# Kernel optimization log

Hardware: AMD Instinct MI355X
Metric: run time of the kernel (lower is better)

Reference implementation:

```python
import jax, jax.numpy as jnp
import numpy as np

C1, C2, BIG_K, STRIDE = 256, 256, 13, 1
EPS = 1e-5  # BatchNorm2d default


def setup_inputs() -> dict:
    key = jax.random.key(0)
    k1, k2, k3, k4, k5 = jax.random.split(key, 5)
    x = jax.random.normal(k1, (16, C1, 56, 56), dtype=jnp.float32)
    # Conv2d weight: (out_ch, in_ch, kH, kW), kaiming-ish scale
    w = jax.random.normal(k2, (C2, C1, BIG_K, BIG_K), dtype=jnp.float32) * (1.0 / np.sqrt(C1 * BIG_K * BIG_K))
    gamma = jax.random.uniform(k3, (C2,), dtype=jnp.float32, minval=0.5, maxval=1.5)
    beta = jax.random.normal(k4, (C2,), dtype=jnp.float32) * 0.1
    running_mean = jnp.zeros((C2,), dtype=jnp.float32)
    running_var = jax.random.uniform(k5, (C2,), dtype=jnp.float32, minval=0.5, maxval=1.5)
    return {"x": x, "w": w, "gamma": gamma, "beta": beta,
            "running_mean": running_mean, "running_var": running_var}


def reference(x, w, gamma, beta, running_mean, running_var):
    # Dense big_k x big_k conv fallback: Conv2d(c1, c2, 13, stride=1, pad=6, bias=False)
    pad = BIG_K // 2
    y = jax.lax.conv_general_dilated(
        x, w,
        window_strides=(STRIDE, STRIDE),
        padding=[(pad, pad), (pad, pad)],
        dimension_numbers=("NCHW", "OIHW", "NCHW"),
    )
    # BatchNorm2d (inference mode: running stats)
    inv = jax.lax.rsqrt(running_var + EPS)
    y = (y - running_mean[None, :, None, None]) * (gamma * inv)[None, :, None, None] + beta[None, :, None, None]
    # SiLU activation
    return y * jax.nn.sigmoid(y)
```

## Files before the change

kernel.cpp:

```cpp
#include <hip/hip_runtime.h>
#include <hip/hip_bf16.h>

#define C1c 256
#define C2c 256
#define NBAT 16
#define HH 56
#define WW 56
#define KS 13
#define PADc 6
#define HP 68
#define NPIX (NBAT*HH*WW)
#define PIXTILES 196
#define KSTEPS2 1352

typedef __bf16 bf16;
typedef bf16 bf16x8 __attribute__((ext_vector_type(8)));
typedef float floatx4 __attribute__((ext_vector_type(4)));

#define XT_ELEMS ((size_t)NBAT*HP*HP*C1c)
#define WT_ELEMS ((size_t)KSTEPS2*256*32)

__global__ __launch_bounds__(256) void xform_x(const float* __restrict__ x,
                                               bf16* __restrict__ xT) {
  __shared__ bf16 tile[56][258];
  const int tid = threadIdx.x;
  const int n = blockIdx.x / HP;
  const int hp = blockIdx.x - n * HP;
  const int ih = hp - PADc;
  const size_t pos_base = (size_t)(n * HP + hp) * HP * C1c;

  if (ih < 0 || ih >= HH) {
#pragma unroll 1
    for (int i = tid; i < HP * 32; i += 256) {
      int wp = i >> 5, g = i & 31;
      *(uint4*)(xT + pos_base + wp * C1c + g * 8) = (uint4){0u, 0u, 0u, 0u};
    }
    return;
  }

  const int wave = tid >> 6, lane = tid & 63;
#pragma unroll 4
  for (int i = 0; i < 64; ++i) {
    int c = i * 4 + wave;
    if (lane < WW) {
      float v = x[(((size_t)n * C1c + c) * HH + ih) * WW + lane];
      tile[lane][c] = (bf16)v;
    }
  }
  __syncthreads();

#pragma unroll 1
  for (int i = tid; i < HP * 32; i += 256) {
    int wp = i >> 5, g = i & 31;
    int iw = wp - PADc;
    uint4 o;
    if (iw >= 0 && iw < WW) {
      const uint* lp = (const uint*)&tile[iw][g * 8];
      o.x = lp[0]; o.y = lp[1]; o.z = lp[2]; o.w = lp[3];
    } else {
      o = (uint4){0u, 0u, 0u, 0u};
    }
    *(uint4*)(xT + pos_base + wp * C1c + g * 8) = o;
  }
}

__global__ __launch_bounds__(256) void xform_w(const float* __restrict__ w,
                                               bf16* __restrict__ wT) {
  int j = blockIdx.x * 256 + threadIdx.x;
  int part = j & 3;
  int c2 = (j >> 2) & 255;
  int kk = j >> 10;
  int kw = kk % 13;
  int t = kk / 13;
  int q = t & 7;
  int kh = t >> 3;
  int c1 = q * 32 + part * 8;
  const float* wp = w + ((size_t)c2 * C1c + c1) * (KS * KS) + kh * KS + kw;
  bf16x8 v;
#pragma unroll
  for (int i = 0; i < 8; i++) v[i] = (bf16)wp[(size_t)i * KS * KS];
  *(bf16x8*)(wT + (size_t)j * 8) = v;
}

__device__ __forceinline__ void gload_lds16(const bf16* g, bf16* l) {
  __builtin_amdgcn_global_load_lds(
      (const __attribute__((address_space(1))) void*)(g),
      (__attribute__((address_space(3))) void*)(l),
      16, 0, 0);
}

__global__ __launch_bounds__(512, 2) void conv_mfma(
    const bf16* __restrict__ xT, const bf16* __restrict__ wT,
    const float* __restrict__ gamma, const float* __restrict__ beta,
    const float* __restrict__ rmean, const float* __restrict__ rvar,
    float* __restrict__ out) {
  __shared__ __attribute__((aligned(16))) bf16 As[3][256 * 32];
  __shared__ __attribute__((aligned(16))) bf16 Bs[3][256 * 32];
  __shared__ float sS[256];
  __shared__ float sB[256];

  const int tid = threadIdx.x;
  const int lane = tid & 63;
  const int wave = tid >> 6;
  const int wm = wave >> 2, wn = wave & 3;

  const int orig = blockIdx.x;
  const int xcd = orig & 7, kb = orig >> 3;
  const int pixt = (xcd < 4 ? xcd * 25 : 100 + (xcd - 4) * 24) + kb;
  const int pixbase = pixt * 256;

  if (tid < 256) {
    float s = gamma[tid] * rsqrtf(rvar[tid] + 1e-5f);
    sS[tid] = s;
    sB[tid] = beta[tid] - rmean[tid] * s;
  }
  __syncthreads();

  const int part = tid & 3;
  const int row0 = tid >> 2;
  const int srcg = (part ^ ((row0 >> 1) & 3)) * 8;

  const int aOff0 = row0 * 32 + srcg;
  const int aOff1 = aOff0 + 128 * 32;

  int pOff0, pOff1;
  {
    int pix = pixbase + row0;
    int n = pix / (HH * WW);
    int rr = pix - n * (HH * WW);
    int oh = rr / WW;
    int ow = rr - oh * WW;
    pOff0 = ((n * HP + oh) * HP + ow) * C1c + srcg;
    pix += 128;
    n = pix / (HH * WW);
    rr = pix - n * (HH * WW);
    oh = rr / WW;
    ow = rr - oh * WW;
    pOff1 = ((n * HP + oh) * HP + ow) * C1c + srcg;
  }

  const int ldsA0 = wave * 512;

  const int mrow = lane & 15;
  const int kq = lane >> 4;
  const int g0 = (kq ^ ((mrow >> 1) & 3)) * 8;
  const int aRB = (wm * 128 + mrow) * 32 + g0;
  const int bRB = (wn * 64 + mrow) * 32 + g0;

  floatx4 acc[8][4];
#pragma unroll
  for (int mi = 0; mi < 8; mi++)
#pragma unroll
    for (int ni = 0; ni < 4; ni++) acc[mi][ni] = (floatx4){0.f, 0.f, 0.f, 0.f};

  gload_lds16(wT + aOff0, &As[0][ldsA0]);
  gload_lds16(wT + aOff1, &As[0][4096 + ldsA0]);
  gload_lds16(xT + pOff0, &Bs[0][ldsA0]);
  gload_lds16(xT + pOff1, &Bs[0][4096 + ldsA0]);
  gload_lds16(wT + 8192 + aOff0, &As[1][ldsA0]);
  gload_lds16(wT + 8192 + aOff1, &As[1][4096 + ldsA0]);
  gload_lds16(xT + pOff0 + C1c, &Bs[1][ldsA0]);
  gload_lds16(xT + pOff1 + C1c, &Bs[1][4096 + ldsA0]);
  asm volatile("s_waitcnt vmcnt(4)" ::: "memory");
  __builtin_amdgcn_s_barrier();

  int kwn = 2, qn = 0, khn = 0;
  const bf16* aPre = wT + 2 * 8192;

  auto do_step = [&](const bf16* Ac, const bf16* Bc, bf16* An, bf16* Bn) {

    bf16x8 af[8], bfr[4];
#pragma unroll
    for (int mi = 0; mi < 4; mi++)
      af[mi] = *(const bf16x8*)(Ac + aRB + mi * 512);
#pragma unroll
    for (int ni = 0; ni < 4; ni++)
      bfr[ni] = *(const bf16x8*)(Bc + bRB + ni * 512);
    gload_lds16(aPre + aOff0, An + ldsA0);
    gload_lds16(aPre + aOff1, An + 4096 + ldsA0);
    __builtin_amdgcn_sched_barrier(0);
    __builtin_amdgcn_s_barrier();
    __builtin_amdgcn_sched_barrier(0);
    __builtin_amdgcn_s_setprio(1);
#pragma unroll
    for (int mi = 0; mi < 4; mi++)
#pragma unroll
      for (int ni = 0; ni < 4; ni++)
        acc[mi][ni] = __builtin_amdgcn_mfma_f32_16x16x32_bf16(
            af[mi], bfr[ni], acc[mi][ni], 0, 0, 0);
    __builtin_amdgcn_s_setprio(0);

#pragma unroll
    for (int mi = 4; mi < 8; mi++)
      af[mi] = *(const bf16x8*)(Ac + aRB + mi * 512);
    int bOn = (khn * HP + kwn) * C1c + qn * 32;
    gload_lds16(xT + pOff0 + bOn, Bn + ldsA0);
    gload_lds16(xT + pOff1 + bOn, Bn + 4096 + ldsA0);
    kwn++; aPre += 8192;
    if (kwn == 13) {
      kwn = 0; qn++;
      if (qn == 8) {
        qn = 0; khn++;
        if (khn == 13) { khn = 0; aPre = wT; }
      }
    }
    __builtin_amdgcn_sched_barrier(0);
    __builtin_amdgcn_s_barrier();
    __builtin_amdgcn_sched_barrier(0);
    __builtin_amdgcn_s_setprio(1);
#pragma unroll
    for (int mi = 4; mi < 8; mi++)
#pragma unroll
      for (int ni = 0; ni < 4; ni++)
        acc[mi][ni] = __builtin_amdgcn_mfma_f32_16x16x32_bf16(
            af[mi], bfr[ni], acc[mi][ni], 0, 0, 0);
    __builtin_amdgcn_s_setprio(0);

    asm volatile("s_waitcnt vmcnt(4)" ::: "memory");
    __builtin_amdgcn_s_barrier();
  };

#pragma unroll 1
  for (int kk = 0; kk < KSTEPS2 - 2; kk += 3) {
    do_step(As[0], Bs[0], As[2], Bs[2]);
    do_step(As[1], Bs[1], As[0], Bs[0]);
    do_step(As[2], Bs[2], As[1], Bs[1]);
  }
  do_step(As[0], Bs[0], As[2], Bs[2]);
  do_step(As[1], Bs[1], As[0], Bs[0]);

  const int colL = lane & 15;
  const int quad = lane >> 4;
#pragma unroll
  for (int ni = 0; ni < 4; ni++) {
    int pix = pixbase + wn * 64 + ni * 16 + colL;
    int n = pix / (HH * WW);
    int rr = pix - n * (HH * WW);
    int oh = rr / WW;
    int ow = rr - oh * WW;
    size_t obase = (size_t)n * C2c * (HH * WW) + (size_t)oh * WW + ow;
#pragma unroll
    for (int mi = 0; mi < 8; mi++) {
      int rowb = wm * 128 + mi * 16 + quad * 4;
#pragma unroll
      for (int r = 0; r < 4; r++) {
        int rowl = rowb + r;
        float v = acc[mi][ni][r];
        v = v * sS[rowl] + sB[rowl];
        float o = v / (1.f + __expf(-v));
        out[obase + (size_t)rowl * (HH * WW)] = o;
      }
    }
  }
}

extern "C" void kernel_launch(void* const* d_in, const int* in_sizes, int n_in,
                              void* d_out, int out_size, void* d_ws, size_t ws_size,
                              hipStream_t stream) {
  const float* x     = (const float*)d_in[0];
  const float* w     = (const float*)d_in[1];
  const float* gamma = (const float*)d_in[2];
  const float* beta  = (const float*)d_in[3];
  const float* rmean = (const float*)d_in[4];
  const float* rvar  = (const float*)d_in[5];
  float* out = (float*)d_out;

  bf16* xT = (bf16*)d_ws;
  bf16* wT = xT + XT_ELEMS;

  if (ws_size < (XT_ELEMS + WT_ELEMS) * sizeof(bf16)) return;

  xform_x<<<NBAT * HP, 256, 0, stream>>>(x, xT);
  xform_w<<<(KSTEPS2 * 256 * 4) / 256, 256, 0, stream>>>(w, wT);
  conv_mfma<<<PIXTILES, 512, 0, stream>>>(xT, wT, gamma, beta, rmean, rvar, out);
}
```

Measured before the change: 1.226 ms.

## Use 224-pixel tiles with 4x2 wave layout to fill all CUs

Changes the pixel tile from 256 to 224 so the grid grows from 196 to 224 blocks, which better matches the 256 CUs. The wave layout moves from 2x4 to 4x2, with each wave computing 64 channels by 112 pixels (4x7 MFMA tiles). Only 7 of the 8 waves stage B, and their vmcnt waits are adjusted to match. This trades per-block arithmetic intensity and a less square per-wave tile for better CU occupancy and less tail imbalance. The XCD-aware block mapping is also simplified.

```diff
diff --git a/kernel.cpp b/kernel.cpp
--- a/kernel.cpp
+++ b/kernel.cpp
@@ -10,7 +10,8 @@
 #define PADc 6
 #define HP 68
 #define NPIX (NBAT*HH*WW)
-#define PIXTILES 196
+#define PIXTILES 224
+#define PTILE 224
 #define KSTEPS2 1352
 
 typedef __bf16 bf16;
@@ -95,19 +96,18 @@
     const float* __restrict__ rmean, const float* __restrict__ rvar,
     float* __restrict__ out) {
   __shared__ __attribute__((aligned(16))) bf16 As[3][256 * 32];
-  __shared__ __attribute__((aligned(16))) bf16 Bs[3][256 * 32];
+  __shared__ __attribute__((aligned(16))) bf16 Bs[3][PTILE * 32];
   __shared__ float sS[256];
   __shared__ float sB[256];
 
   const int tid = threadIdx.x;
   const int lane = tid & 63;
   const int wave = tid >> 6;
-  const int wm = wave >> 2, wn = wave & 3;
+  const int wm = wave >> 1, wn = wave & 1;
 
   const int orig = blockIdx.x;
-  const int xcd = orig & 7, kb = orig >> 3;
-  const int pixt = (xcd < 4 ? xcd * 25 : 100 + (xcd - 4) * 24) + kb;
-  const int pixbase = pixt * 256;
+  const int pixt = (orig & 7) * 28 + (orig >> 3);
+  const int pixbase = pixt * PTILE;
 
   if (tid < 256) {
     float s = gamma[tid] * rsqrtf(rvar[tid] + 1e-5f);
@@ -123,15 +123,16 @@
   const int aOff0 = row0 * 32 + srcg;
   const int aOff1 = aOff0 + 128 * 32;
 
-  int pOff0, pOff1;
-  {
+  const bool bstage = (wave < 7);
+  int pOff0 = 0, pOff1 = 0;
+  if (bstage) {
     int pix = pixbase + row0;
     int n = pix / (HH * WW);
     int rr = pix - n * (HH * WW);
     int oh = rr / WW;
     int ow = rr - oh * WW;
     pOff0 = ((n * HP + oh) * HP + ow) * C1c + srcg;
-    pix += 128;
+    pix += 112;
     n = pix / (HH * WW);
     rr = pix - n * (HH * WW);
     oh = rr / WW;
@@ -140,41 +141,46 @@
   }
 
   const int ldsA0 = wave * 512;
+  const int ldsB1 = 112 * 32 + wave * 512;
 
   const int mrow = lane & 15;
   const int kq = lane >> 4;
   const int g0 = (kq ^ ((mrow >> 1) & 3)) * 8;
-  const int aRB = (wm * 128 + mrow) * 32 + g0;
-  const int bRB = (wn * 64 + mrow) * 32 + g0;
-
-  floatx4 acc[8][4];
-#pragma unroll
-  for (int mi = 0; mi < 8; mi++)
-#pragma unroll
-    for (int ni = 0; ni < 4; ni++) acc[mi][ni] = (floatx4){0.f, 0.f, 0.f, 0.f};
+  const int aRB = (wm * 64 + mrow) * 32 + g0;
+  const int bRB = (wn * 112 + mrow) * 32 + g0;
+
+  floatx4 acc[4][7];
+#pragma unroll
+  for (int mi = 0; mi < 4; mi++)
+#pragma unroll
+    for (int ni = 0; ni < 7; ni++) acc[mi][ni] = (floatx4){0.f, 0.f, 0.f, 0.f};
 
   gload_lds16(wT + aOff0, &As[0][ldsA0]);
   gload_lds16(wT + aOff1, &As[0][4096 + ldsA0]);
-  gload_lds16(xT + pOff0, &Bs[0][ldsA0]);
-  gload_lds16(xT + pOff1, &Bs[0][4096 + ldsA0]);
+  if (bstage) {
+    gload_lds16(xT + pOff0, &Bs[0][ldsA0]);
+    gload_lds16(xT + pOff1, &Bs[0][ldsB1]);
+  }
   gload_lds16(wT + 8192 + aOff0, &As[1][ldsA0]);
   gload_lds16(wT + 8192 + aOff1, &As[1][4096 + ldsA0]);
-  gload_lds16(xT + pOff0 + C1c, &Bs[1][ldsA0]);
-  gload_lds16(xT + pOff1 + C1c, &Bs[1][4096 + ldsA0]);
-  asm volatile("s_waitcnt vmcnt(4)" ::: "memory");
+  if (bstage) {
+    gload_lds16(xT + pOff0 + C1c, &Bs[1][ldsA0]);
+    gload_lds16(xT + pOff1 + C1c, &Bs[1][ldsB1]);
+  }
+  if (bstage) { asm volatile("s_waitcnt vmcnt(4)" ::: "memory"); }
+  else        { asm volatile("s_waitcnt vmcnt(2)" ::: "memory"); }
   __builtin_amdgcn_s_barrier();
 
   int kwn = 2, qn = 0, khn = 0;
   const bf16* aPre = wT + 2 * 8192;
 
   auto do_step = [&](const bf16* Ac, const bf16* Bc, bf16* An, bf16* Bn) {
-
-    bf16x8 af[8], bfr[4];
-#pragma unroll
-    for (int mi = 0; mi < 4; mi++)
+    bf16x8 af[4], bfr[7];
+#pragma unroll
+    for (int mi = 0; mi < 2; mi++)
       af[mi] = *(const bf16x8*)(Ac + aRB + mi * 512);
 #pragma unroll
-    for (int ni = 0; ni < 4; ni++)
+    for (int ni = 0; ni < 7; ni++)
       bfr[ni] = *(const bf16x8*)(Bc + bRB + ni * 512);
     gload_lds16(aPre + aOff0, An + ldsA0);
     gload_lds16(aPre + aOff1, An + 4096 + ldsA0);
@@ -183,19 +189,21 @@
     __builtin_amdgcn_sched_barrier(0);
     __builtin_amdgcn_s_setprio(1);
 #pragma unroll
-    for (int mi = 0; mi < 4; mi++)
-#pragma unroll
-      for (int ni = 0; ni < 4; ni++)
+    for (int mi = 0; mi < 2; mi++)
+#pragma unroll
+      for (int ni = 0; ni < 7; ni++)
         acc[mi][ni] = __builtin_amdgcn_mfma_f32_16x16x32_bf16(
             af[mi], bfr[ni], acc[mi][ni], 0, 0, 0);
     __builtin_amdgcn_s_setprio(0);
 
 #pragma unroll
-    for (int mi = 4; mi < 8; mi++)
+    for (int mi = 2; mi < 4; mi++)
       af[mi] = *(const bf16x8*)(Ac + aRB + mi * 512);
     int bOn = (khn * HP + kwn) * C1c + qn * 32;
-    gload_lds16(xT + pOff0 + bOn, Bn + ldsA0);
-    gload_lds16(xT + pOff1 + bOn, Bn + 4096 + ldsA0);
+    if (bstage) {
+      gload_lds16(xT + pOff0 + bOn, Bn + ldsA0);
+      gload_lds16(xT + pOff1 + bOn, Bn + ldsB1);
+    }
     kwn++; aPre += 8192;
     if (kwn == 13) {
       kwn = 0; qn++;
@@ -209,14 +217,15 @@
     __builtin_amdgcn_sched_barrier(0);
     __builtin_amdgcn_s_setprio(1);
 #pragma unroll
-    for (int mi = 4; mi < 8; mi++)
-#pragma unroll
-      for (int ni = 0; ni < 4; ni++)
+    for (int mi = 2; mi < 4; mi++)
+#pragma unroll
+      for (int ni = 0; ni < 7; ni++)
         acc[mi][ni] = __builtin_amdgcn_mfma_f32_16x16x32_bf16(
             af[mi], bfr[ni], acc[mi][ni], 0, 0, 0);
     __builtin_amdgcn_s_setprio(0);
 
-    asm volatile("s_waitcnt vmcnt(4)" ::: "memory");
+    if (bstage) { asm volatile("s_waitcnt vmcnt(4)" ::: "memory"); }
+    else        { asm volatile("s_waitcnt vmcnt(2)" ::: "memory"); }
     __builtin_amdgcn_s_barrier();
   };
 
@@ -232,16 +241,16 @@
   const int colL = lane & 15;
   const int quad = lane >> 4;
 #pragma unroll
-  for (int ni = 0; ni < 4; ni++) {
-    int pix = pixbase + wn * 64 + ni * 16 + colL;
+  for (int ni = 0; ni < 7; ni++) {
+    int pix = pixbase + wn * 112 + ni * 16 + colL;
     int n = pix / (HH * WW);
     int rr = pix - n * (HH * WW);
     int oh = rr / WW;
     int ow = rr - oh * WW;
     size_t obase = (size_t)n * C2c * (HH * WW) + (size_t)oh * WW + ow;
 #pragma unroll
-    for (int mi = 0; mi < 8; mi++) {
-      int rowb = wm * 128 + mi * 16 + quad * 4;
+    for (int mi = 0; mi < 4; mi++) {
+      int rowb = wm * 64 + mi * 16 + quad * 4;
 #pragma unroll
       for (int r = 0; r < 4; r++) {
         int rowl = rowb + r;
```

Result: no change. 1.217 ms (-0.7%).
